# Kernel tuning notes

Measured on AMD Instinct MI355X. Metric: run time of the kernel, lower is better.

The kernel has to match this reference:

```python
import jax, jax.numpy as jnp
import numpy as np

TOPIC = 128
HID = 128
K = 50
N_HIST = 200000
DECAY = 1.0 - 1e-07


def setup_inputs() -> dict:
    key = jax.random.key(0)
    ks = jax.random.split(key, 12)
    return {
        "v": jax.random.normal(ks[0], (TOPIC,), jnp.float32),
        "s": jax.random.uniform(ks[1], (1,), jnp.float32),
        "t": jnp.ones((1,), jnp.float32),
        "vs": jax.random.normal(ks[2], (N_HIST, TOPIC), jnp.float32),
        "hs": jax.random.normal(ks[3], (N_HIST, 1, HID), jnp.float32),
        "ts": jax.random.uniform(ks[4], (N_HIST,), jnp.float32),
        "W_ih": jax.random.normal(ks[5], (3 * HID, TOPIC + 1), jnp.float32) * 0.05,
        "b_ih": jax.random.normal(ks[6], (3 * HID,), jnp.float32) * 0.05,
        "W_hh": jax.random.normal(ks[7], (3 * HID, HID), jnp.float32) * 0.05,
        "b_hh": jax.random.normal(ks[8], (3 * HID,), jnp.float32) * 0.05,
        "W_score": jax.random.normal(ks[9], (1, TOPIC + HID), jnp.float32) * 0.05,
        "b_score": jax.random.normal(ks[10], (1,), jnp.float32) * 0.05,
    }


def reference(v, s, t, vs, hs, ts, W_ih, b_ih, W_hh, b_hh, W_score, b_score):
    N, _, H = hs.shape
    # --- time-decayed top-k similarity attention over stored history ---
    ts_delta = t - ts                                  # [N]
    alpha = vs @ v                                     # [N] similarity scores
    alpha_k, idx = jax.lax.top_k(alpha, K)             # top-k (order-invariant downstream)
    alpha_k = alpha_k * DECAY ** ts_delta[idx]         # elementwise time decay
    w = jax.nn.softmax(alpha_k)                        # [K]
    hs_flat = hs.reshape(N, H)                         # num_layers=1
    attn_h = w @ hs_flat[idx]                          # [H] weighted sum of gathered states
    # --- score head ---
    pred_v = jnp.concatenate([v, attn_h])[None, :]     # [1, TOPIC+H]
    score = pred_v @ W_score.T + b_score               # [1, 1]
    # --- single GRU step (torch gate order: r, z, n) ---
    x = jnp.concatenate([v, s])                        # [TOPIC+1] (concat score_mode)
    h0 = hs_flat[-1]                                   # last hidden state [H]
    gi = x @ W_ih.T + b_ih                             # [3H]
    gh = h0 @ W_hh.T + b_hh                            # [3H]
    i_r, i_z, i_n = jnp.split(gi, 3)
    h_r, h_z, h_n = jnp.split(gh, 3)
    r = jax.nn.sigmoid(i_r + h_r)
    z = jax.nn.sigmoid(i_z + h_z)
    n = jnp.tanh(i_n + r * h_n)
    h_new = (1.0 - z) * n + z * h0                     # [H]
    return score, h_new.reshape(1, 1, H)
```

## Files before the change

### kernel.cpp

```cpp
#include <hip/hip_runtime.h>
#include <math.h>

#define N_HIST 200000
#define TOPIC 128
#define HID 128
#define KSEL 50
#define NBINS 4096
#define NHISTBLK 64
#define NCOLLECT 128
#define NGRUBLK 96
#define NMID (NCOLLECT + NGRUBLK)
#define NPOOL 32
#define POOL_CAP 256
#define NEG_INF (-3.402823466e38f)
#define LOG_DECAY (-1.1920930e-07f)

enum { WS_CTRL  = 0,
       WS_TOT   = 64,
       WS_HIST2 = WS_TOT + NBINS,
       WS_ZEND  = WS_HIST2 + 2048,
       WS_ALPHA = WS_ZEND,
       WS_POOLV = WS_ALPHA + N_HIST,
       WS_POOLI = WS_POOLV + NPOOL * POOL_CAP,
       WS_GI    = WS_POOLI + NPOOL * POOL_CAP,
       WS_GH    = WS_GI + 3 * HID };

__device__ __forceinline__ unsigned keyOf(float f) {
    unsigned u = __float_as_uint(f);
    return (u & 0x80000000u) ? ~u : (u | 0x80000000u);
}

__global__ __launch_bounds__(256) void alpha_kernel(
        const float* __restrict__ vs, const float* __restrict__ v,
        float* __restrict__ alpha, unsigned* __restrict__ wsbase) {
    const int zi = blockIdx.x * 256 + threadIdx.x;
    if (zi < WS_ZEND) wsbase[zi] = 0;
    const int lane = threadIdx.x & 63;
    const int wave = (blockIdx.x * blockDim.x + threadIdx.x) >> 6;
    const int half = lane >> 5;
    const int c = lane & 31;
    const int base = wave * 16 + half * 8;
    const float4 vv = ((const float4*)v)[c];
    float4 a[8];
    #pragma unroll
    for (int r = 0; r < 8; ++r)
        a[r] = ((const float4*)vs)[(size_t)(base + r) * 32 + c];
    float s[8];
    #pragma unroll
    for (int r = 0; r < 8; ++r)
        s[r] = a[r].x * vv.x + a[r].y * vv.y + a[r].z * vv.z + a[r].w * vv.w;
    #pragma unroll
    for (int off = 16; off; off >>= 1) {
        #pragma unroll
        for (int r = 0; r < 8; ++r) s[r] += __shfl_xor(s[r], off);
    }
    if (c == 0) {
        float4* dst = (float4*)(alpha + base);
        dst[0] = make_float4(s[0], s[1], s[2], s[3]);
        dst[1] = make_float4(s[4], s[5], s[6], s[7]);
    }
}

__global__ __launch_bounds__(256) void hist_kernel(
        const float* __restrict__ alpha, unsigned* __restrict__ tot,
        unsigned* __restrict__ ctrl) {
    __shared__ unsigned h[NBINS / 2];
    __shared__ unsigned lt[NBINS];
    __shared__ int sLast;
    const int t = threadIdx.x;
    #pragma unroll
    for (int i = t; i < NBINS / 2; i += 256) h[i] = 0;
    __syncthreads();
    const float4* a4 = (const float4*)alpha;
    for (int i4 = blockIdx.x * 256 + t; i4 < N_HIST / 4; i4 += NHISTBLK * 256) {
        float4 av = a4[i4];
        #pragma unroll
        for (int r = 0; r < 4; ++r) {
            unsigned b = keyOf((&av.x)[r]) >> 20;
            atomicAdd(&h[b >> 1], (b & 1u) ? 65536u : 1u);
        }
    }
    __syncthreads();
    #pragma unroll
    for (int wd = t; wd < NBINS / 2; wd += 256) {
        unsigned pk = h[wd];
        unsigned lo = pk & 0xFFFFu, hi = pk >> 16;
        if (lo) atomicAdd(&tot[2 * wd], lo);
        if (hi) atomicAdd(&tot[2 * wd + 1], hi);
    }
    __syncthreads();
    if (t == 0) {
        __threadfence();
        sLast = (atomicAdd(&ctrl[0], 1u) == NHISTBLK - 1) ? 1 : 0;
    }
    __syncthreads();
    if (sLast) {
        __threadfence();
        #pragma unroll
        for (int i = t; i < NBINS; i += 256) lt[i] = tot[i];
        __syncthreads();
        if (t < 64) {
            const int l = t;
            const int g = 63 - l;
            unsigned s = 0;
            #pragma unroll
            for (int j = 0; j < 64; ++j) s += lt[g * 64 + j];
            unsigned pre = s;
            #pragma unroll
            for (int d = 1; d <= 32; d <<= 1) {
                unsigned y = __shfl_up(pre, d);
                if (l >= d) pre += y;
            }
            unsigned long long bal = __ballot(pre >= KSEL);
            const int lstar = __ffsll(bal) - 1;
            const unsigned cumAbove = __shfl(pre - s, lstar);
            const int gstar = 63 - lstar;
            unsigned h2 = lt[gstar * 64 + (63 - l)];
            unsigned pre2 = h2;
            #pragma unroll
            for (int d = 1; d <= 32; d <<= 1) {
                unsigned y = __shfl_up(pre2, d);
                if (l >= d) pre2 += y;
            }
            unsigned long long bal2 = __ballot(cumAbove + pre2 >= KSEL);
            const int l2 = __ffsll(bal2) - 1;
            if (l == 0) ctrl[2] = (unsigned)(gstar * 64 + (63 - l2));
        }
    }
}

__global__ __launch_bounds__(256) void mid_kernel(
        const float* __restrict__ alpha, unsigned* __restrict__ ctrl,
        unsigned* __restrict__ hist2g,
        float* __restrict__ poolV, unsigned* __restrict__ poolI,
        const float* __restrict__ v, const float* __restrict__ s_in,
        const float* __restrict__ t_in,
        const float* __restrict__ hs, const float* __restrict__ ts,
        const float* __restrict__ W_ih, const float* __restrict__ b_ih,
        const float* __restrict__ W_hh, const float* __restrict__ b_hh,
        const float* __restrict__ W_score, const float* __restrict__ b_score,
        float* __restrict__ giW, float* __restrict__ ghW,
        float* __restrict__ out) {
    __shared__ unsigned pcnt[NPOOL];
    __shared__ unsigned selCnt, eqCnt, sB2;
    __shared__ int sLast;
    __shared__ float selV[64];
    __shared__ unsigned selI[64];
    __shared__ float eqV[256];
    __shared__ unsigned eqI[256];
    __shared__ float w[64];
    __shared__ float xv[TOPIC];
    __shared__ float h0[HID];
    __shared__ float attnP[4][130];
    __shared__ float red[HID];

    const int t = threadIdx.x;
    const int wv = t >> 6, l = t & 63;

    if (blockIdx.x < NCOLLECT) {
        const unsigned B = ctrl[2];
        const int pool = blockIdx.x & (NPOOL - 1);
        const float4* a4 = (const float4*)alpha;
        for (int i4 = blockIdx.x * 256 + t; i4 < N_HIST / 4; i4 += NCOLLECT * 256) {
            float4 av = a4[i4];
            #pragma unroll
            for (int r = 0; r < 4; ++r) {
                float a = (&av.x)[r];
                unsigned k = keyOf(a);
                unsigned top = k >> 20;
                bool cand = top >= B;
                unsigned long long m = __ballot(cand);
                if (m) {
                    int leader = __ffsll(m) - 1;
                    unsigned base = 0;
                    if (l == leader) base = atomicAdd(&ctrl[8 + pool], (unsigned)__popcll(m));
                    base = __shfl(base, leader);
                    if (cand) {
                        unsigned pos = base + (unsigned)__popcll(m & ((1ull << l) - 1ull));
                        if (pos < POOL_CAP) {
                            poolV[pool * POOL_CAP + pos] = a;
                            poolI[pool * POOL_CAP + pos] = (unsigned)(4 * i4 + r);
                        }
                        if (top > B) atomicAdd(&ctrl[3], 1u);
                        else atomicAdd(&hist2g[(k >> 9) & 2047], 1u);
                    }
                }
            }
        }
    } else {
        const int o = ((int)blockIdx.x - NCOLLECT) * 4 + wv;
        const float* wi = W_ih + (size_t)o * (TOPIC + 1);
        float pi = wi[l] * v[l] + wi[64 + l] * v[64 + l];
        if (l == 0) pi += wi[TOPIC] * s_in[0];
        const float2 wh = ((const float2*)(W_hh + (size_t)o * HID))[l];
        const float2 hh = ((const float2*)(hs + (size_t)(N_HIST - 1) * HID))[l];
        float ph = wh.x * hh.x + wh.y * hh.y;
        #pragma unroll
        for (int off = 32; off; off >>= 1) {
            pi += __shfl_xor(pi, off);
            ph += __shfl_xor(ph, off);
        }
        if (l == 0) {
            giW[o] = pi + b_ih[o];
            ghW[o] = ph + b_hh[o];
        }
    }

    __syncthreads();
    if (t == 0) {
        __threadfence();
        sLast = (atomicAdd(&ctrl[1], 1u) == NMID - 1) ? 1 : 0;
    }
    __syncthreads();
    if (!sLast) return;
    __threadfence();

    const unsigned B = ctrl[2];
    const unsigned cHi = ctrl[3];

    if (wv == 0) {
        const int g = 63 - l;
        const uint4* h4 = (const uint4*)(hist2g + g * 32);
        unsigned s = 0;
        #pragma unroll
        for (int j = 0; j < 8; ++j) { uint4 q = h4[j]; s += q.x + q.y + q.z + q.w; }
        unsigned pre = s;
        #pragma unroll
        for (int d = 1; d <= 32; d <<= 1) {
            unsigned y = __shfl_up(pre, d);
            if (l >= d) pre += y;
        }
        unsigned long long bal = __ballot(cHi + pre >= KSEL);
        const int lstar = __ffsll(bal) - 1;
        const unsigned cumAbove = cHi + __shfl(pre - s, lstar);
        const int gstar = 63 - lstar;
        unsigned h2 = (l < 32) ? hist2g[gstar * 32 + (31 - l)] : 0u;
        unsigned pre2 = h2;
        #pragma unroll
        for (int d = 1; d <= 16; d <<= 1) {
            unsigned y = __shfl_up(pre2, d);
            if (l >= d) pre2 += y;
        }
        unsigned long long bal2 = __ballot((l < 32) && (cumAbove + pre2 >= KSEL));
        const int l2 = __ffsll(bal2) - 1;
        if (l == 0) sB2 = (unsigned)(gstar * 32 + (31 - l2));
    } else {
        if (t >= 64 && t < 96) pcnt[t - 64] = min(ctrl[8 + (t - 64)], (unsigned)POOL_CAP);
        if (t == 96) { selCnt = 0; eqCnt = 0; }
        if (t >= 128 && t < 256) h0[t - 128] = hs[(size_t)(N_HIST - 1) * HID + (t - 128)];
    }
    __syncthreads();
    const unsigned B2 = sB2;

    {
        const int p = t >> 3, i0 = t & 7;
        const int cnt = (int)pcnt[p];
        for (int i = i0; i < cnt; i += 8) {
            float a = poolV[p * POOL_CAP + i];
            unsigned k = keyOf(a);
            unsigned top = k >> 20, sub = (k >> 9) & 2047;
            bool hi = (top > B) || (top == B && sub > B2);
            bool eq = (top == B) && (sub == B2);
            if (hi) {
                unsigned pos = atomicAdd(&selCnt, 1u);
                if (pos < 64u) { selV[pos] = a; selI[pos] = poolI[p * POOL_CAP + i]; }
            } else if (eq) {
                unsigned pos = atomicAdd(&eqCnt, 1u);
                if (pos < 256u) { eqV[pos] = a; eqI[pos] = poolI[p * POOL_CAP + i]; }
            }
        }
    }
    __syncthreads();

    const int Scnt = min((int)selCnt, 64);
    const int eqN = min((int)eqCnt, 256);
    int need = KSEL - Scnt;
    if (need < 0) need = 0;
    if (need > eqN) need = eqN;
    const int S = Scnt + need;

    if (wv == 0) {
        if (need > 0) {
            for (int c = l; c < eqN; c += 64) {
                const float mv = eqV[c];
                const unsigned mi = eqI[c];
                int r = 0;
                for (int j = 0; j < eqN; ++j) {
                    const float vj = eqV[j];
                    const unsigned ij = eqI[j];
                    r += (int)((vj > mv) | ((vj == mv) & (ij < mi)));
                }
                if (r < need) { selV[Scnt + r] = mv; selI[Scnt + r] = mi; }
            }
        }
    } else if (t >= 128 && t < 256) {
        xv[t - 128] = v[t - 128];
    }
    __syncthreads();

    unsigned ridx[13];
    float2 hv[13];
    #pragma unroll
    for (int j = 0; j < 13; ++j) {
        const int k = wv + 4 * j;
        ridx[j] = (k < S) ? selI[k] : 0u;
    }
    #pragma unroll
    for (int j = 0; j < 13; ++j)
        hv[j] = ((const float2*)(hs + (size_t)ridx[j] * HID))[l];

    if (wv == 0) {
        const float tt = t_in[0];
        float dv = NEG_INF;
        if (l < S) dv = selV[l] * expf((tt - ts[selI[l]]) * LOG_DECAY);
        float m = dv;
        #pragma unroll
        for (int o = 32; o; o >>= 1) m = fmaxf(m, __shfl_xor(m, o));
        float e = (l < S) ? expf(dv - m) : 0.f;
        float sum = e;
        #pragma unroll
        for (int o = 32; o; o >>= 1) sum += __shfl_xor(sum, o);
        if (l < S) w[l] = e / sum;
    }
    __syncthreads();

    {
        float2 acc = make_float2(0.f, 0.f);
        #pragma unroll
        for (int j = 0; j < 13; ++j) {
            const int k = wv + 4 * j;
            const float wk = (k < S) ? w[k] : 0.f;
            acc.x += wk * hv[j].x; acc.y += wk * hv[j].y;
        }
        attnP[wv][2 * l]     = acc.x;
        attnP[wv][2 * l + 1] = acc.y;
    }
    __syncthreads();

    if (t < HID) {
        float ah = attnP[0][t] + attnP[1][t] + attnP[2][t] + attnP[3][t];
        red[t] = xv[t] * W_score[t] + ah * W_score[HID + t];
        const float r = 1.f / (1.f + expf(-(giW[t] + ghW[t])));
        const float z = 1.f / (1.f + expf(-(giW[HID + t] + ghW[HID + t])));
        const float n = tanhf(giW[2 * HID + t] + r * ghW[2 * HID + t]);
        out[1 + t] = (1.f - z) * n + z * h0[t];
    }
    __syncthreads();

    if (t < 64) {
        float sv = red[t] + red[64 + t];
        #pragma unroll
        for (int o = 32; o; o >>= 1) sv += __shfl_xor(sv, o);
        if (t == 0) out[0] = sv + b_score[0];
    }
}

extern "C" void kernel_launch(void* const* d_in, const int* in_sizes, int n_in,
                              void* d_out, int out_size, void* d_ws, size_t ws_size,
                              hipStream_t stream) {
    const float* v       = (const float*)d_in[0];
    const float* s_in    = (const float*)d_in[1];
    const float* t_in    = (const float*)d_in[2];
    const float* vs      = (const float*)d_in[3];
    const float* hs      = (const float*)d_in[4];
    const float* ts      = (const float*)d_in[5];
    const float* W_ih    = (const float*)d_in[6];
    const float* b_ih    = (const float*)d_in[7];
    const float* W_hh    = (const float*)d_in[8];
    const float* b_hh    = (const float*)d_in[9];
    const float* W_score = (const float*)d_in[10];
    const float* b_score = (const float*)d_in[11];
    float* out = (float*)d_out;

    unsigned* ws     = (unsigned*)d_ws;
    unsigned* ctrl   = ws + WS_CTRL;
    unsigned* tot    = ws + WS_TOT;
    unsigned* hist2g = ws + WS_HIST2;
    float*    alpha  = (float*)(ws + WS_ALPHA);
    float*    poolV  = (float*)(ws + WS_POOLV);
    unsigned* poolI  = ws + WS_POOLI;
    float*    giW    = (float*)(ws + WS_GI);
    float*    ghW    = (float*)(ws + WS_GH);

    alpha_kernel<<<3125, 256, 0, stream>>>(vs, v, alpha, ws);
    hist_kernel<<<NHISTBLK, 256, 0, stream>>>(alpha, tot, ctrl);
    mid_kernel<<<NMID, 256, 0, stream>>>(alpha, ctrl, hist2g, poolV, poolI,
                                         v, s_in, t_in, hs, ts,
                                         W_ih, b_ih, W_hh, b_hh, W_score, b_score,
                                         giW, ghW, out);
}
```

Measured before the change: 42.52 us.

## Fuse alpha, histogram and candidate collection into one persistent kernel

Merges the three kernels into a single 512-block kernel. Each block computes its dot-product scores and keeps them in shared memory, builds the coarse histogram, then waits on a global flag spin barrier for the threshold bin before collecting candidates from shared memory. This removes the 200K-float alpha buffer round trip and two kernel launch boundaries. In exchange it relies on all 512 blocks being co-resident for the spin-wait to avoid deadlock, and it adds a hipMemsetAsync for zeroing the workspace.

```diff
diff --git a/kernel.cpp b/kernel.cpp
--- a/kernel.cpp
+++ b/kernel.cpp
@@ -6,12 +6,12 @@
 #define HID 128
 #define KSEL 50
 #define NBINS 4096
-#define NHISTBLK 64
-#define NCOLLECT 128
-#define NGRUBLK 96
-#define NMID (NCOLLECT + NGRUBLK)
+#define NBLK 512
+#define NWAVE (NBLK * 4)
+#define NGRP (N_HIST / 16)
 #define NPOOL 32
 #define POOL_CAP 256
+#define GRU0 96
 #define NEG_INF (-3.402823466e38f)
 #define LOG_DECAY (-1.1920930e-07f)
 
@@ -19,8 +19,7 @@
        WS_TOT   = 64,
        WS_HIST2 = WS_TOT + NBINS,
        WS_ZEND  = WS_HIST2 + 2048,
-       WS_ALPHA = WS_ZEND,
-       WS_POOLV = WS_ALPHA + N_HIST,
+       WS_POOLV = WS_ZEND,
        WS_POOLI = WS_POOLV + NPOOL * POOL_CAP,
        WS_GI    = WS_POOLI + NPOOL * POOL_CAP,
        WS_GH    = WS_GI + 3 * HID };
@@ -30,77 +29,112 @@
     return (u & 0x80000000u) ? ~u : (u | 0x80000000u);
 }
 
-__global__ __launch_bounds__(256) void alpha_kernel(
+__global__ __launch_bounds__(256, 2) void fused_kernel(
         const float* __restrict__ vs, const float* __restrict__ v,
-        float* __restrict__ alpha, unsigned* __restrict__ wsbase) {
-    const int zi = blockIdx.x * 256 + threadIdx.x;
-    if (zi < WS_ZEND) wsbase[zi] = 0;
-    const int lane = threadIdx.x & 63;
-    const int wave = (blockIdx.x * blockDim.x + threadIdx.x) >> 6;
-    const int half = lane >> 5;
-    const int c = lane & 31;
-    const int base = wave * 16 + half * 8;
-    const float4 vv = ((const float4*)v)[c];
-    float4 a[8];
-    #pragma unroll
-    for (int r = 0; r < 8; ++r)
-        a[r] = ((const float4*)vs)[(size_t)(base + r) * 32 + c];
-    float s[8];
-    #pragma unroll
-    for (int r = 0; r < 8; ++r)
-        s[r] = a[r].x * vv.x + a[r].y * vv.y + a[r].z * vv.z + a[r].w * vv.w;
-    #pragma unroll
-    for (int off = 16; off; off >>= 1) {
-        #pragma unroll
-        for (int r = 0; r < 8; ++r) s[r] += __shfl_xor(s[r], off);
-    }
-    if (c == 0) {
-        float4* dst = (float4*)(alpha + base);
-        dst[0] = make_float4(s[0], s[1], s[2], s[3]);
-        dst[1] = make_float4(s[4], s[5], s[6], s[7]);
-    }
-}
-
-__global__ __launch_bounds__(256) void hist_kernel(
-        const float* __restrict__ alpha, unsigned* __restrict__ tot,
-        unsigned* __restrict__ ctrl) {
+        const float* __restrict__ s_in, const float* __restrict__ t_in,
+        const float* __restrict__ hs, const float* __restrict__ ts,
+        const float* __restrict__ W_ih, const float* __restrict__ b_ih,
+        const float* __restrict__ W_hh, const float* __restrict__ b_hh,
+        const float* __restrict__ W_score, const float* __restrict__ b_score,
+        unsigned* __restrict__ ctrl, unsigned* __restrict__ tot,
+        unsigned* __restrict__ hist2g,
+        float* __restrict__ poolV, unsigned* __restrict__ poolI,
+        float* __restrict__ giW, float* __restrict__ ghW,
+        float* __restrict__ out) {
     __shared__ unsigned h[NBINS / 2];
+    __shared__ float chunkV[7][4][16];
     __shared__ unsigned lt[NBINS];
-    __shared__ int sLast;
+    __shared__ int sLast1, sLast2;
+    __shared__ unsigned pcnt[NPOOL];
+    __shared__ unsigned selCnt, eqCnt, sB2, sCHi;
+    __shared__ float selV[64];
+    __shared__ unsigned selI[64];
+    __shared__ float eqV[256];
+    __shared__ unsigned eqI[256];
+    __shared__ float w[64];
+    __shared__ float xv[TOPIC];
+    __shared__ float h0[HID];
+    __shared__ float attnP[4][130];
+    __shared__ float red[HID];
+
     const int t = threadIdx.x;
-    #pragma unroll
+    const int wv = t >> 6, l = t & 63;
+    const int blk = blockIdx.x;
+
     for (int i = t; i < NBINS / 2; i += 256) h[i] = 0;
     __syncthreads();
-    const float4* a4 = (const float4*)alpha;
-    for (int i4 = blockIdx.x * 256 + t; i4 < N_HIST / 4; i4 += NHISTBLK * 256) {
-        float4 av = a4[i4];
-        #pragma unroll
-        for (int r = 0; r < 4; ++r) {
-            unsigned b = keyOf((&av.x)[r]) >> 20;
-            atomicAdd(&h[b >> 1], (b & 1u) ? 65536u : 1u);
-        }
-    }
-    __syncthreads();
-    #pragma unroll
+
+    {
+        const int half = l >> 5, c = l & 31;
+        const int wave = blk * 4 + wv;
+        const float4 vv = ((const float4*)v)[c];
+        #pragma unroll
+        for (int i = 0; i < 7; ++i) {
+            const int g = wave + NWAVE * i;
+            if (g < NGRP) {
+                const int base = g * 16 + half * 8;
+                float4 a[8];
+                #pragma unroll
+                for (int r = 0; r < 8; ++r)
+                    a[r] = ((const float4*)vs)[(size_t)(base + r) * 32 + c];
+                float s[8];
+                #pragma unroll
+                for (int r = 0; r < 8; ++r)
+                    s[r] = a[r].x * vv.x + a[r].y * vv.y + a[r].z * vv.z + a[r].w * vv.w;
+                #pragma unroll
+                for (int off = 16; off; off >>= 1) {
+                    #pragma unroll
+                    for (int r = 0; r < 8; ++r) s[r] += __shfl_xor(s[r], off);
+                }
+                if (c == 0) {
+                    #pragma unroll
+                    for (int r = 0; r < 8; ++r) {
+                        chunkV[i][wv][half * 8 + r] = s[r];
+                        unsigned b = keyOf(s[r]) >> 20;
+                        atomicAdd(&h[b >> 1], (b & 1u) ? 65536u : 1u);
+                    }
+                }
+            }
+        }
+    }
+    __syncthreads();
+
     for (int wd = t; wd < NBINS / 2; wd += 256) {
         unsigned pk = h[wd];
-        unsigned lo = pk & 0xFFFFu, hi = pk >> 16;
+        unsigned lo = pk & 0xFFFFu, hi2 = pk >> 16;
         if (lo) atomicAdd(&tot[2 * wd], lo);
-        if (hi) atomicAdd(&tot[2 * wd + 1], hi);
-    }
-    __syncthreads();
-    if (t == 0) {
+        if (hi2) atomicAdd(&tot[2 * wd + 1], hi2);
+    }
+    __threadfence();
+    __syncthreads();
+    if (t == 0) sLast1 = (atomicAdd(&ctrl[1], 1u) == NBLK - 1) ? 1 : 0;
+    __syncthreads();
+
+    if (blk >= GRU0 && blk < GRU0 + 96) {
+        const int o = (blk - GRU0) * 4 + wv;
+        const float* wi = W_ih + (size_t)o * (TOPIC + 1);
+        float pi = wi[l] * v[l] + wi[64 + l] * v[64 + l];
+        if (l == 0) pi += wi[TOPIC] * s_in[0];
+        const float2 wh = ((const float2*)(W_hh + (size_t)o * HID))[l];
+        const float2 hh = ((const float2*)(hs + (size_t)(N_HIST - 1) * HID))[l];
+        float ph = wh.x * hh.x + wh.y * hh.y;
+        #pragma unroll
+        for (int off = 32; off; off >>= 1) {
+            pi += __shfl_xor(pi, off);
+            ph += __shfl_xor(ph, off);
+        }
+        if (l == 0) {
+            giW[o] = pi + b_ih[o];
+            ghW[o] = ph + b_hh[o];
+        }
         __threadfence();
-        sLast = (atomicAdd(&ctrl[0], 1u) == NHISTBLK - 1) ? 1 : 0;
-    }
-    __syncthreads();
-    if (sLast) {
+    }
+
+    if (sLast1) {
         __threadfence();
-        #pragma unroll
         for (int i = t; i < NBINS; i += 256) lt[i] = tot[i];
         __syncthreads();
         if (t < 64) {
-            const int l = t;
             const int g = 63 - l;
             unsigned s = 0;
             #pragma unroll
@@ -126,97 +160,60 @@
             const int l2 = __ffsll(bal2) - 1;
             if (l == 0) ctrl[2] = (unsigned)(gstar * 64 + (63 - l2));
         }
-    }
-}
-
-__global__ __launch_bounds__(256) void mid_kernel(
-        const float* __restrict__ alpha, unsigned* __restrict__ ctrl,
-        unsigned* __restrict__ hist2g,
-        float* __restrict__ poolV, unsigned* __restrict__ poolI,
-        const float* __restrict__ v, const float* __restrict__ s_in,
-        const float* __restrict__ t_in,
-        const float* __restrict__ hs, const float* __restrict__ ts,
-        const float* __restrict__ W_ih, const float* __restrict__ b_ih,
-        const float* __restrict__ W_hh, const float* __restrict__ b_hh,
-        const float* __restrict__ W_score, const float* __restrict__ b_score,
-        float* __restrict__ giW, float* __restrict__ ghW,
-        float* __restrict__ out) {
-    __shared__ unsigned pcnt[NPOOL];
-    __shared__ unsigned selCnt, eqCnt, sB2;
-    __shared__ int sLast;
-    __shared__ float selV[64];
-    __shared__ unsigned selI[64];
-    __shared__ float eqV[256];
-    __shared__ unsigned eqI[256];
-    __shared__ float w[64];
-    __shared__ float xv[TOPIC];
-    __shared__ float h0[HID];
-    __shared__ float attnP[4][130];
-    __shared__ float red[HID];
-
-    const int t = threadIdx.x;
-    const int wv = t >> 6, l = t & 63;
-
-    if (blockIdx.x < NCOLLECT) {
-        const unsigned B = ctrl[2];
-        const int pool = blockIdx.x & (NPOOL - 1);
-        const float4* a4 = (const float4*)alpha;
-        for (int i4 = blockIdx.x * 256 + t; i4 < N_HIST / 4; i4 += NCOLLECT * 256) {
-            float4 av = a4[i4];
-            #pragma unroll
-            for (int r = 0; r < 4; ++r) {
-                float a = (&av.x)[r];
-                unsigned k = keyOf(a);
-                unsigned top = k >> 20;
-                bool cand = top >= B;
-                unsigned long long m = __ballot(cand);
-                if (m) {
-                    int leader = __ffsll(m) - 1;
-                    unsigned base = 0;
-                    if (l == leader) base = atomicAdd(&ctrl[8 + pool], (unsigned)__popcll(m));
-                    base = __shfl(base, leader);
-                    if (cand) {
-                        unsigned pos = base + (unsigned)__popcll(m & ((1ull << l) - 1ull));
-                        if (pos < POOL_CAP) {
-                            poolV[pool * POOL_CAP + pos] = a;
-                            poolI[pool * POOL_CAP + pos] = (unsigned)(4 * i4 + r);
-                        }
-                        if (top > B) atomicAdd(&ctrl[3], 1u);
-                        else atomicAdd(&hist2g[(k >> 9) & 2047], 1u);
-                    }
+        __syncthreads();
+        if (t == 0) { __threadfence(); atomicExch(&ctrl[4], 1u); }
+    } else {
+        if (t == 0) {
+            while (atomicAdd(&ctrl[4], 0u) == 0u) __builtin_amdgcn_s_sleep(2);
+        }
+    }
+    __syncthreads();
+    if (t == 0) sCHi = atomicAdd(&ctrl[2], 0u);
+    __syncthreads();
+    const unsigned B = sCHi;
+
+    #pragma unroll
+    for (int rep = 0; rep < 2; ++rep) {
+        const int j = t + rep * 256;
+        const int i = j >> 6, wv2 = (j >> 4) & 3, r = j & 15;
+        float a = 0.f;
+        int g = 0;
+        bool inb = (j < 448);
+        if (inb) {
+            g = (blk * 4 + wv2) + NWAVE * i;
+            if (g < NGRP) a = chunkV[i][wv2][r];
+            else inb = false;
+        }
+        const unsigned k = keyOf(a);
+        const bool cand = inb && ((k >> 20) >= B);
+        unsigned long long m = __ballot(cand);
+        if (m) {
+            const int pool = blk & (NPOOL - 1);
+            int leader = __ffsll(m) - 1;
+            unsigned basep = 0;
+            if (l == leader) basep = atomicAdd(&ctrl[8 + pool], (unsigned)__popcll(m));
+            basep = __shfl(basep, leader);
+            if (cand) {
+                unsigned pos = basep + (unsigned)__popcll(m & ((1ull << l) - 1ull));
+                if (pos < POOL_CAP) {
+                    poolV[pool * POOL_CAP + pos] = a;
+                    poolI[pool * POOL_CAP + pos] = (unsigned)(g * 16 + r);
                 }
-            }
-        }
-    } else {
-        const int o = ((int)blockIdx.x - NCOLLECT) * 4 + wv;
-        const float* wi = W_ih + (size_t)o * (TOPIC + 1);
-        float pi = wi[l] * v[l] + wi[64 + l] * v[64 + l];
-        if (l == 0) pi += wi[TOPIC] * s_in[0];
-        const float2 wh = ((const float2*)(W_hh + (size_t)o * HID))[l];
-        const float2 hh = ((const float2*)(hs + (size_t)(N_HIST - 1) * HID))[l];
-        float ph = wh.x * hh.x + wh.y * hh.y;
-        #pragma unroll
-        for (int off = 32; off; off >>= 1) {
-            pi += __shfl_xor(pi, off);
-            ph += __shfl_xor(ph, off);
-        }
-        if (l == 0) {
-            giW[o] = pi + b_ih[o];
-            ghW[o] = ph + b_hh[o];
-        }
-    }
-
-    __syncthreads();
-    if (t == 0) {
-        __threadfence();
-        sLast = (atomicAdd(&ctrl[1], 1u) == NMID - 1) ? 1 : 0;
-    }
-    __syncthreads();
-    if (!sLast) return;
+                if ((k >> 20) > B) atomicAdd(&ctrl[3], 1u);
+                else atomicAdd(&hist2g[(k >> 9) & 2047], 1u);
+            }
+        }
+    }
     __threadfence();
-
-    const unsigned B = ctrl[2];
-    const unsigned cHi = ctrl[3];
+    __syncthreads();
+    if (t == 0) sLast2 = (atomicAdd(&ctrl[5], 1u) == NBLK - 1) ? 1 : 0;
+    __syncthreads();
+    if (!sLast2) return;
+    __threadfence();
+
+    if (t == 0) sCHi = atomicAdd(&ctrl[3], 0u);
+    __syncthreads();
+    const unsigned cHi = sCHi;
 
     if (wv == 0) {
         const int g = 63 - l;
@@ -376,16 +373,14 @@
     unsigned* ctrl   = ws + WS_CTRL;
     unsigned* tot    = ws + WS_TOT;
     unsigned* hist2g = ws + WS_HIST2;
-    float*    alpha  = (float*)(ws + WS_ALPHA);
     float*    poolV  = (float*)(ws + WS_POOLV);
     unsigned* poolI  = ws + WS_POOLI;
     float*    giW    = (float*)(ws + WS_GI);
     float*    ghW    = (float*)(ws + WS_GH);
 
-    alpha_kernel<<<3125, 256, 0, stream>>>(vs, v, alpha, ws);
-    hist_kernel<<<NHISTBLK, 256, 0, stream>>>(alpha, tot, ctrl);
-    mid_kernel<<<NMID, 256, 0, stream>>>(alpha, ctrl, hist2g, poolV, poolI,
-                                         v, s_in, t_in, hs, ts,
-                                         W_ih, b_ih, W_hh, b_hh, W_score, b_score,
-                                         giW, ghW, out);
+    hipMemsetAsync(ws, 0, (size_t)WS_ZEND * 4, stream);
+    fused_kernel<<<NBLK, 256, 0, stream>>>(vs, v, s_in, t_in, hs, ts,
+                                           W_ih, b_ih, W_hh, b_hh, W_score, b_score,
+                                           ctrl, tot, hist2g, poolV, poolI,
+                                           giW, ghW, out);
 }
```

After: 118.5 us. 2.79x slower.
